# Optimization experiments

Measured on AMD Instinct MI355X. Metric: run time of the kernel, lower is better.

The kernel has to match this reference:

```python
import jax, jax.numpy as jnp
import numpy as np

B, R, D, P = 32, 512, 256, 5532  # images, rois/image, feat dim, num_pids
NEG_INF = -1e30

def setup_inputs() -> dict:
    key = jax.random.key(0)
    k1, k2, k3 = jax.random.split(key, 3)
    inputs = jax.random.normal(k1, (B * R, D), dtype=jnp.float32)
    cls_scores = jax.random.uniform(k2, (B * R, 1), dtype=jnp.float32)
    roi_label = jax.random.randint(k3, (B, R), 0, P + 1)  # 0 = background -> label -1
    return {"inputs": inputs, "cls_scores": cls_scores, "roi_label": roi_label}

def reference(inputs, cls_scores, roi_label):
    x = (inputs * cls_scores).reshape(B, R, D)          # scale features by cls score
    label = roi_label - 1                               # [B,R], -1 = background
    valid = label >= 0                                  # keep labeled ROIs only
    lbl = jnp.where(valid, label, 0)

    # per-image per-pid mean prototypes via one segmented reduction
    seg = (jnp.arange(B)[:, None] * P + lbl).reshape(-1)             # [B*R]
    w = valid.reshape(-1).astype(x.dtype)
    sums = jax.ops.segment_sum(x.reshape(-1, D) * w[:, None], seg, num_segments=B * P)
    counts = jax.ops.segment_sum(w, seg, num_segments=B * P)          # [B*P]
    proto = sums / jnp.maximum(counts, 1.0)[:, None]
    proto = proto / jnp.maximum(jnp.linalg.norm(proto, axis=-1, keepdims=True), 1e-12)
    proto = jax.lax.stop_gradient(proto).reshape(B, P, D)            # .detach() in torch
    present = (counts > 0).reshape(B, P)                              # unique labels per image

    # project each ROI feature onto its image's prototypes
    logits = jnp.einsum('brd,bpd->brp', x, proto)                     # [B,R,P]
    logits = jnp.where(present[:, None, :], logits, NEG_INF)          # softmax over unique labels only
    logp = jax.nn.log_softmax(logits, axis=-1)
    nll = -jnp.take_along_axis(logp, lbl[..., None], axis=-1)[..., 0] # [B,R]
    nll = jnp.where(valid, nll, 0.0)
    n_valid = jnp.maximum(jnp.sum(valid).astype(x.dtype), 1.0)
    return jnp.sum(nll) / n_valid
```

## Files before the change

### kernel.cpp

```cpp
#include <hip/hip_runtime.h>
#include <math.h>

#define Bn 32
#define Rn 512
#define Dn 256
#define Pn 5532
#define MAXU 512

typedef short short8 __attribute__((ext_vector_type(8)));
typedef short short4v __attribute__((ext_vector_type(4)));
typedef float floatx4 __attribute__((ext_vector_type(4)));

#define XBF_OFF    0
#define XBF_WORDS  (Bn*Rn*Dn/2)
#define PBF_OFF    (XBF_OFF + XBF_WORDS)
#define PBF_WORDS  (Bn*MAXU*Dn/2)
#define LBLC_OFF   (PBF_OFF + PBF_WORDS)
#define CCNT_OFF   (LBLC_OFF + Bn*Rn)
#define CURS_OFF   (CCNT_OFF + Bn*MAXU)
#define RLIST_OFF  (CURS_OFF + Bn*MAXU)
#define NUNIQ_OFF  (RLIST_OFF + Bn*Rn)
#define NVALID_OFF (NUNIQ_OFF + 32)
#define SEXP_OFF   (NVALID_OFF + 32)
#define NLL_OFF    (SEXP_OFF + Bn*Rn)
#define TK2_OFF    (NLL_OFF + 1)
#define TICK_OFF   (TK2_OFF + 1)
#define ZEROW      (Bn*Rn + 2 + 128)

__device__ __forceinline__ unsigned short bf16r(float f) {
    union { float f; unsigned int u; } c; c.f = f;
    return (unsigned short)((c.u + 0x7FFFu + ((c.u >> 16) & 1u)) >> 16);
}
__device__ __forceinline__ float bfu2f(unsigned int hi16) {
    union { unsigned int u; float f; } c; c.u = hi16;
    return c.f;
}

__device__ __forceinline__ void async16(void* lds, const void* g) {
    auto* l3 = reinterpret_cast<__attribute__((address_space(3))) unsigned int*>(
                   reinterpret_cast<size_t>(lds));
    auto* g1 = reinterpret_cast<const __attribute__((address_space(1))) unsigned int*>(
                   reinterpret_cast<size_t>(g));
    __builtin_amdgcn_global_load_lds(g1, l3, 16, 0, 0);
}

__global__ __launch_bounds__(1024) void k1_prep(
    const float* __restrict__ inputs, const float* __restrict__ cls,
    const int* __restrict__ roi_label,
    unsigned short* __restrict__ xbf,
    int* __restrict__ lblc_arr, int* __restrict__ ccnt, int* __restrict__ cursor,
    int* __restrict__ rlist, int* __restrict__ nuniq, int* __restrict__ nvalid_arr,
    int* __restrict__ zbase)
{
    const int flat = blockIdx.x;
    const int t = threadIdx.x;

    __shared__ int cnt_lds[Pn];
    __shared__ int cmap_lds[Pn];
    __shared__ int curs_lds[MAXU];
    __shared__ int wpres[16], wcnt[16];

    if (flat >= 32) {
        if (flat >= 33 && flat <= 49) {
            int idx = (flat - 33) * 1024 + t;
            if (idx < ZEROW) zbase[idx] = 0;
        }
        int g = (flat - 32) * 1024 + t;
        int e = g * 8;
        int row = e >> 8;
        float cw = cls[row];
        float4 v0 = *(const float4*)&inputs[e];
        float4 v1 = *(const float4*)&inputs[e + 4];
        short8 o;
        o[0] = (short)bf16r(v0.x * cw); o[1] = (short)bf16r(v0.y * cw);
        o[2] = (short)bf16r(v0.z * cw); o[3] = (short)bf16r(v0.w * cw);
        o[4] = (short)bf16r(v1.x * cw); o[5] = (short)bf16r(v1.y * cw);
        o[6] = (short)bf16r(v1.z * cw); o[7] = (short)bf16r(v1.w * cw);
        *(short8*)&xbf[e] = o;
        return;
    }

    const int b = flat;
    const int lane = t & 63, wid = t >> 6;
    for (int i = t; i < Pn; i += 1024) cnt_lds[i] = 0;
    __syncthreads();
    int mylbl = -1;
    if (t < Rn) {
        mylbl = roi_label[b * Rn + t] - 1;
        if (mylbl >= 0) atomicAdd(&cnt_lds[mylbl], 1);
    }
    __syncthreads();

    int basePres = 0, baseCnt = 0;
    for (int i0 = 0; i0 < Pn; i0 += 1024) {
        int i = i0 + t;
        int cnt = (i < Pn) ? cnt_lds[i] : 0;
        bool pres = cnt > 0;
        unsigned long long mask = __ballot(pres);
        int pfx_pres = __popcll(mask & ((1ULL << lane) - 1ULL));
        int v = cnt;
        #pragma unroll
        for (int off = 1; off < 64; off <<= 1) {
            int u = __shfl_up(v, off);
            if (lane >= off) v += u;
        }
        int pfx_cnt = v - cnt;
        if (lane == 63) { wpres[wid] = __popcll(mask); wcnt[wid] = v; }
        __syncthreads();
        int woffP = 0, totP = 0, woffC = 0, totC = 0;
        #pragma unroll
        for (int w = 0; w < 16; ++w) {
            int p = wpres[w], c = wcnt[w];
            if (w < wid) { woffP += p; woffC += c; }
            totP += p; totC += c;
        }
        if (pres) {
            int c = basePres + woffP + pfx_pres;
            cmap_lds[i] = c;
            ccnt[b * MAXU + c] = cnt;
            curs_lds[c] = baseCnt + woffC + pfx_cnt;
        }
        basePres += totP; baseCnt += totC;
        __syncthreads();
    }
    if (t < Rn) {
        int lc = (mylbl >= 0) ? cmap_lds[mylbl] : -1;
        lblc_arr[b * Rn + t] = lc;
        if (lc >= 0) {
            int pos = atomicAdd(&curs_lds[lc], 1);
            rlist[b * Rn + pos] = t;
        }
    }
    __syncthreads();
    if (t < MAXU && t < basePres)
        cursor[b * MAXU + t] = curs_lds[t];
    if (t == 0) { nuniq[b] = basePres; nvalid_arr[b] = baseCnt; }
}

__global__ __launch_bounds__(256) void k2_proto(
    const unsigned short* __restrict__ xbf,
    const int* __restrict__ nuniq, const int* __restrict__ ccnt,
    const int* __restrict__ cursor, const int* __restrict__ rlist,
    unsigned short* __restrict__ pbf)
{
    const int lane = threadIdx.x & 63, wv = threadIdx.x >> 6;
    int s = blockIdx.x * 4 + wv;
    int b = s >> 9;
    int c = s & (MAXU - 1);
    if (c >= nuniq[b]) return;
    int cnt = ccnt[s];
    int start = cursor[s] - cnt;
    float a0 = 0.f, a1 = 0.f, a2 = 0.f, a3 = 0.f;
    for (int k = 0; k < cnt; ++k) {
        int r = rlist[b * Rn + start + k];
        uint2 pk = *(const uint2*)&xbf[((size_t)(b * Rn + r)) * Dn + lane * 4];
        a0 += bfu2f(pk.x << 16); a1 += bfu2f(pk.x & 0xFFFF0000u);
        a2 += bfu2f(pk.y << 16); a3 += bfu2f(pk.y & 0xFFFF0000u);
    }
    float inv = 1.0f / (float)cnt;
    a0 *= inv; a1 *= inv; a2 *= inv; a3 *= inv;
    float ss = a0*a0 + a1*a1 + a2*a2 + a3*a3;
    #pragma unroll
    for (int off = 32; off > 0; off >>= 1) ss += __shfl_xor(ss, off);
    float scale = 1.0f / fmaxf(sqrtf(ss), 1e-12f);
    short4v o;
    o[0] = (short)bf16r(a0 * scale); o[1] = (short)bf16r(a1 * scale);
    o[2] = (short)bf16r(a2 * scale); o[3] = (short)bf16r(a3 * scale);
    *(short4v*)&pbf[(size_t)s * Dn + lane * 4] = o;
}

#define TRr 128
#define TCc 128
#define KCk 32

__global__ __launch_bounds__(256, 3) void k3_loss(
    const unsigned short* __restrict__ xbf, const unsigned short* __restrict__ pbf,
    const int* __restrict__ lblc_arr, const int* __restrict__ nuniq,
    float* __restrict__ sexp, float* __restrict__ nll,
    int* __restrict__ tick, int* __restrict__ ticket2,
    const int* __restrict__ nvalid_arr, float* __restrict__ out)
{
    __shared__ __align__(16) unsigned short xs[2][TRr * KCk];
    __shared__ __align__(16) unsigned short ps[2][TCc * KCk];
    __shared__ int lblc[TRr];
    __shared__ float msum[4];
    __shared__ int mflag;

    const int t = threadIdx.x;
    const int lane = t & 63, w = t >> 6;
    const int q = lane >> 4, r15 = lane & 15;
    const int rt = blockIdx.x;
    const int b = blockIdx.y;
    const int pc = blockIdx.z;
    const int roiBase = rt * TRr;
    const int U = nuniq[b];
    const int nch = (U == 0) ? 1 : ((U + TCc - 1) >> 7);
    if (pc >= nch) return;

    if (t < TRr) lblc[t] = lblc_arr[b * Rn + roiBase + t];

    int xrow[2], xg[2];
    #pragma unroll
    for (int cc = 0; cc < 2; ++cc) {
        int s = (w + cc * 4) * 64 + lane;
        xrow[cc] = s >> 2; xg[cc] = (s & 3) ^ ((xrow[cc] >> 1) & 3);
    }

    #define ISSUE(kc, buf)                                                         \
        do {                                                                       \
            async16(&xs[buf][w * 512],                                             \
                    xbf + (size_t)(b * Rn + roiBase + xrow[0]) * Dn                \
                        + (kc) * KCk + xg[0] * 8);                                 \
            async16(&xs[buf][(w + 4) * 512],                                       \
                    xbf + (size_t)(b * Rn + roiBase + xrow[1]) * Dn                \
                        + (kc) * KCk + xg[1] * 8);                                 \
            async16(&ps[buf][w * 512],                                             \
                    pbf + (size_t)(b * MAXU + pc * TCc + xrow[0]) * Dn             \
                        + (kc) * KCk + xg[0] * 8);                                 \
            async16(&ps[buf][(w + 4) * 512],                                       \
                    pbf + (size_t)(b * MAXU + pc * TCc + xrow[1]) * Dn             \
                        + (kc) * KCk + xg[1] * 8);                                 \
        } while (0)

    ISSUE(0, 0);

    floatx4 acc[8][2];
    #pragma unroll
    for (int mt = 0; mt < 8; ++mt)
        #pragma unroll
        for (int nt = 0; nt < 2; ++nt) acc[mt][nt] = (floatx4)0.f;

    for (int kc = 0; kc < Dn / KCk; ++kc) {
        const int cur = kc & 1;
        __syncthreads();
        if (kc < Dn / KCk - 1) ISSUE(kc + 1, cur ^ 1);

        short8 bb[2];
        #pragma unroll
        for (int nt = 0; nt < 2; ++nt) {
            int row = w * 32 + nt * 16 + r15;
            int off = row * KCk + ((q ^ ((row >> 1) & 3)) * 8);
            bb[nt] = *(const short8*)&ps[cur][off];
        }
        #pragma unroll
        for (int mt = 0; mt < 8; ++mt) {
            int row = mt * 16 + r15;
            int off = row * KCk + ((q ^ ((row >> 1) & 3)) * 8);
            short8 a = *(const short8*)&xs[cur][off];
            acc[mt][0] = __builtin_amdgcn_mfma_f32_16x16x32_bf16(a, bb[0], acc[mt][0], 0, 0, 0);
            acc[mt][1] = __builtin_amdgcn_mfma_f32_16x16x32_bf16(a, bb[1], acc[mt][1], 0, 0, 0);
        }
    }
    #undef ISSUE

    const int c0 = pc * TCc + w * 32 + r15;
    const int c1 = c0 + 16;
    const bool v0 = c0 < U, v1 = c1 < U;
    float dsum = 0.f;
    #pragma unroll
    for (int mt = 0; mt < 8; ++mt)
        #pragma unroll
        for (int reg = 0; reg < 4; ++reg) {
            int mloc = mt * 16 + q * 4 + reg;
            float d0 = acc[mt][0][reg], d1 = acc[mt][1][reg];
            int lc = lblc[mloc];
            if (v0 && c0 == lc) dsum += d0;
            if (v1 && c1 == lc) dsum += d1;
            float es = (v0 ? __expf(d0) : 0.f) + (v1 ? __expf(d1) : 0.f);
            #pragma unroll
            for (int off = 1; off < 16; off <<= 1) es += __shfl_xor(es, off);
            if (r15 == 0) atomicAdd(&sexp[b * Rn + roiBase + mloc], es);
        }
    #pragma unroll
    for (int off = 1; off < 64; off <<= 1) dsum += __shfl_xor(dsum, off);
    if (lane == 0) msum[w] = dsum;
    __syncthreads();
    if (t == 0) {
        atomicAdd(nll, -(msum[0] + msum[1] + msum[2] + msum[3]));
        __threadfence();
        int old = atomicAdd(&tick[b * 4 + rt], 1);
        mflag = (old == nch - 1);
    }
    __syncthreads();
    if (mflag) {
        float v = 0.f;
        if (t < TRr && lblc[t] >= 0)
            v = __logf(atomicAdd(&sexp[b * Rn + roiBase + t], 0.0f));
        #pragma unroll
        for (int off = 1; off < 64; off <<= 1) v += __shfl_xor(v, off);
        if (lane == 0) msum[w] = v;
        __syncthreads();
        if (t == 0) {
            atomicAdd(nll, msum[0] + msum[1] + msum[2] + msum[3]);
            __threadfence();
            int t2 = atomicAdd(ticket2, 1);
            if (t2 == 127) {
                float total = atomicAdd(nll, 0.0f);
                int nv = 0;
                for (int bb2 = 0; bb2 < Bn; ++bb2) nv += nvalid_arr[bb2];
                out[0] = total / fmaxf((float)nv, 1.0f);
            }
        }
    }
}

extern "C" void kernel_launch(void* const* d_in, const int* in_sizes, int n_in,
                              void* d_out, int out_size, void* d_ws, size_t ws_size,
                              hipStream_t stream) {
    const float* inputs = (const float*)d_in[0];
    const float* cls    = (const float*)d_in[1];
    const int*   roi    = (const int*)d_in[2];
    float* out = (float*)d_out;

    float* wsf = (float*)d_ws;
    int*   wsi = (int*)d_ws;
    unsigned short* xbf = (unsigned short*)(wsi + XBF_OFF);
    unsigned short* pbf = (unsigned short*)(wsi + PBF_OFF);
    int*   lblc   = wsi + LBLC_OFF;
    int*   ccnt   = wsi + CCNT_OFF;
    int*   cursor = wsi + CURS_OFF;
    int*   rlist  = wsi + RLIST_OFF;
    int*   nuniq  = wsi + NUNIQ_OFF;
    int*   nvalid = wsi + NVALID_OFF;
    float* sexp   = wsf + SEXP_OFF;
    float* nll    = wsf + NLL_OFF;
    int*   tk2    = wsi + TK2_OFF;
    int*   tick   = wsi + TICK_OFF;

    k1_prep<<<32 + 512, 1024, 0, stream>>>(inputs, cls, roi, xbf, lblc, ccnt,
                                           cursor, rlist, nuniq, nvalid,
                                           wsi + SEXP_OFF);
    k2_proto<<<(Bn * MAXU) / 4, 256, 0, stream>>>(xbf, nuniq, ccnt, cursor,
                                                  rlist, pbf);
    dim3 g(Rn / TRr, Bn, 4);
    k3_loss<<<g, 256, 0, stream>>>(xbf, pbf, lblc, nuniq, sexp, nll, tick, tk2,
                                   nvalid, out);
}
```

Before: 103.4 us.

## Restructure loss kernel to loop over prototype chunks with register-resident ROI tiles

The loss kernel now assigns each block 32 ROIs and loops over all prototype chunks itself, instead of splitting chunks across grid z. ROI features are loaded once into LDS and held in registers, and only prototype tiles are double-buffered. Row-wise exp sums and target logits accumulate in registers, which removes the global sexp array, its per-row atomics, the second ticket pass and most of the workspace zeroing. In exchange each block repeats the prototype loads for every 32 ROIs, and blocks for images with many unique labels run longer serial loops.

```diff
diff --git a/kernel.cpp b/kernel.cpp
--- a/kernel.cpp
+++ b/kernel.cpp
@@ -21,11 +21,9 @@
 #define RLIST_OFF  (CURS_OFF + Bn*MAXU)
 #define NUNIQ_OFF  (RLIST_OFF + Bn*Rn)
 #define NVALID_OFF (NUNIQ_OFF + 32)
-#define SEXP_OFF   (NVALID_OFF + 32)
-#define NLL_OFF    (SEXP_OFF + Bn*Rn)
-#define TK2_OFF    (NLL_OFF + 1)
-#define TICK_OFF   (TK2_OFF + 1)
-#define ZEROW      (Bn*Rn + 2 + 128)
+#define NLL_OFF    (NVALID_OFF + 32)
+#define TICK_OFF   (NLL_OFF + 1)
+#define ZEROW      2
 
 __device__ __forceinline__ unsigned short bf16r(float f) {
     union { float f; unsigned int u; } c; c.f = f;
@@ -61,10 +59,7 @@
     __shared__ int wpres[16], wcnt[16];
 
     if (flat >= 32) {
-        if (flat >= 33 && flat <= 49) {
-            int idx = (flat - 33) * 1024 + t;
-            if (idx < ZEROW) zbase[idx] = 0;
-        }
+        if (flat == 33 && t < ZEROW) zbase[t] = 0;
         int g = (flat - 32) * 1024 + t;
         int e = g * 8;
         int row = e >> 8;
@@ -169,135 +164,163 @@
     *(short4v*)&pbf[(size_t)s * Dn + lane * 4] = o;
 }
 
-#define TRr 128
+#define TRr 32
 #define TCc 128
-#define KCk 32
+#define KCs 64
+#define NSTG (Dn / KCs)
+#define NBLK ((Rn / TRr) * Bn)
 
 __global__ __launch_bounds__(256, 3) void k3_loss(
     const unsigned short* __restrict__ xbf, const unsigned short* __restrict__ pbf,
     const int* __restrict__ lblc_arr, const int* __restrict__ nuniq,
-    float* __restrict__ sexp, float* __restrict__ nll,
-    int* __restrict__ tick, int* __restrict__ ticket2,
-    const int* __restrict__ nvalid_arr, float* __restrict__ out)
+    const int* __restrict__ nvalid_arr,
+    float* __restrict__ nll, int* __restrict__ tick, float* __restrict__ out)
 {
-    __shared__ __align__(16) unsigned short xs[2][TRr * KCk];
-    __shared__ __align__(16) unsigned short ps[2][TCc * KCk];
+    __shared__ __align__(16) unsigned short xs[TRr * Dn];
+    __shared__ __align__(16) unsigned short ps[2][TCc * KCs];
     __shared__ int lblc[TRr];
-    __shared__ float msum[4];
-    __shared__ int mflag;
+    __shared__ float esum_lds[4][TRr];
+    __shared__ float dsum_lds[4][TRr];
 
     const int t = threadIdx.x;
     const int lane = t & 63, w = t >> 6;
     const int q = lane >> 4, r15 = lane & 15;
     const int rt = blockIdx.x;
-    const int b = blockIdx.y;
-    const int pc = blockIdx.z;
+    const int b  = blockIdx.y;
     const int roiBase = rt * TRr;
     const int U = nuniq[b];
-    const int nch = (U == 0) ? 1 : ((U + TCc - 1) >> 7);
-    if (pc >= nch) return;
+    const int nch = (U <= 0) ? 1 : ((U + TCc - 1) >> 7);
 
     if (t < TRr) lblc[t] = lblc_arr[b * Rn + roiBase + t];
 
-    int xrow[2], xg[2];
-    #pragma unroll
-    for (int cc = 0; cc < 2; ++cc) {
-        int s = (w + cc * 4) * 64 + lane;
-        xrow[cc] = s >> 2; xg[cc] = (s & 3) ^ ((xrow[cc] >> 1) & 3);
-    }
-
-    #define ISSUE(kc, buf)                                                         \
-        do {                                                                       \
-            async16(&xs[buf][w * 512],                                             \
-                    xbf + (size_t)(b * Rn + roiBase + xrow[0]) * Dn                \
-                        + (kc) * KCk + xg[0] * 8);                                 \
-            async16(&xs[buf][(w + 4) * 512],                                       \
-                    xbf + (size_t)(b * Rn + roiBase + xrow[1]) * Dn                \
-                        + (kc) * KCk + xg[1] * 8);                                 \
-            async16(&ps[buf][w * 512],                                             \
-                    pbf + (size_t)(b * MAXU + pc * TCc + xrow[0]) * Dn             \
-                        + (kc) * KCk + xg[0] * 8);                                 \
-            async16(&ps[buf][(w + 4) * 512],                                       \
-                    pbf + (size_t)(b * MAXU + pc * TCc + xrow[1]) * Dn             \
-                        + (kc) * KCk + xg[1] * 8);                                 \
-        } while (0)
-
-    ISSUE(0, 0);
-
-    floatx4 acc[8][2];
-    #pragma unroll
-    for (int mt = 0; mt < 8; ++mt)
-        #pragma unroll
-        for (int nt = 0; nt < 2; ++nt) acc[mt][nt] = (floatx4)0.f;
-
-    for (int kc = 0; kc < Dn / KCk; ++kc) {
-        const int cur = kc & 1;
-        __syncthreads();
-        if (kc < Dn / KCk - 1) ISSUE(kc + 1, cur ^ 1);
-
-        short8 bb[2];
+    #pragma unroll
+    for (int i = 0; i < 4; ++i) {
+        int ci = i * 256 + w * 64 + lane;
+        int row = ci >> 5, gpos = ci & 31;
+        int g = gpos ^ (row & 7);
+        async16(&xs[(i * 256 + w * 64) * 8],
+                xbf + (size_t)(b * Rn + roiBase + row) * Dn + g * 8);
+    }
+
+#define ISSUE_PS(PC, ST, BUF)                                                \
+    do {                                                                     \
+        _Pragma("unroll")                                                    \
+        for (int i_ = 0; i_ < 4; ++i_) {                                     \
+            int ci_ = i_ * 256 + w * 64 + lane;                              \
+            int pr_ = ci_ >> 3, gp_ = ci_ & 7;                               \
+            int g_ = gp_ ^ (pr_ & 7);                                        \
+            async16(&ps[BUF][(i_ * 256 + w * 64) * 8],                       \
+                    pbf + (size_t)(b * MAXU + (PC) * TCc + pr_) * Dn         \
+                        + (ST) * KCs + g_ * 8);                              \
+        }                                                                    \
+    } while (0)
+
+    ISSUE_PS(0, 0, 0);
+    __syncthreads();
+
+    short8 areg[2][8];
+    #pragma unroll
+    for (int mt = 0; mt < 2; ++mt)
+        #pragma unroll
+        for (int kcs = 0; kcs < 8; ++kcs) {
+            int row = mt * 16 + r15;
+            int gpos = (kcs * 4 + q) ^ (row & 7);
+            areg[mt][kcs] = *(const short8*)&xs[row * Dn + gpos * 8];
+        }
+
+    int lcr[2][4];
+    float esum[2][4], dsum[2][4];
+    #pragma unroll
+    for (int mt = 0; mt < 2; ++mt)
+        #pragma unroll
+        for (int reg = 0; reg < 4; ++reg) {
+            lcr[mt][reg] = lblc[mt * 16 + q * 4 + reg];
+            esum[mt][reg] = 0.f; dsum[mt][reg] = 0.f;
+        }
+
+    for (int pc = 0; pc < nch; ++pc) {
+        floatx4 acc[2][2];
+        #pragma unroll
+        for (int mt = 0; mt < 2; ++mt) {
+            acc[mt][0] = (floatx4)0.f; acc[mt][1] = (floatx4)0.f;
+        }
+
+        #pragma unroll
+        for (int st = 0; st < NSTG; ++st) {
+            const int cur = st & 1;
+            __syncthreads();
+            int ns = pc * NSTG + st + 1;
+            if (ns < nch * NSTG) ISSUE_PS(ns >> 2, ns & 3, cur ^ 1);
+            #pragma unroll
+            for (int kk = 0; kk < 2; ++kk) {
+                short8 bb[2];
+                #pragma unroll
+                for (int nt = 0; nt < 2; ++nt) {
+                    int r = w * 32 + nt * 16 + r15;
+                    int gpos = (kk * 4 + q) ^ (r & 7);
+                    bb[nt] = *(const short8*)&ps[cur][r * KCs + gpos * 8];
+                }
+                #pragma unroll
+                for (int mt = 0; mt < 2; ++mt) {
+                    acc[mt][0] = __builtin_amdgcn_mfma_f32_16x16x32_bf16(
+                        areg[mt][st * 2 + kk], bb[0], acc[mt][0], 0, 0, 0);
+                    acc[mt][1] = __builtin_amdgcn_mfma_f32_16x16x32_bf16(
+                        areg[mt][st * 2 + kk], bb[1], acc[mt][1], 0, 0, 0);
+                }
+            }
+        }
+
         #pragma unroll
         for (int nt = 0; nt < 2; ++nt) {
-            int row = w * 32 + nt * 16 + r15;
-            int off = row * KCk + ((q ^ ((row >> 1) & 3)) * 8);
-            bb[nt] = *(const short8*)&ps[cur][off];
-        }
-        #pragma unroll
-        for (int mt = 0; mt < 8; ++mt) {
-            int row = mt * 16 + r15;
-            int off = row * KCk + ((q ^ ((row >> 1) & 3)) * 8);
-            short8 a = *(const short8*)&xs[cur][off];
-            acc[mt][0] = __builtin_amdgcn_mfma_f32_16x16x32_bf16(a, bb[0], acc[mt][0], 0, 0, 0);
-            acc[mt][1] = __builtin_amdgcn_mfma_f32_16x16x32_bf16(a, bb[1], acc[mt][1], 0, 0, 0);
-        }
-    }
-    #undef ISSUE
-
-    const int c0 = pc * TCc + w * 32 + r15;
-    const int c1 = c0 + 16;
-    const bool v0 = c0 < U, v1 = c1 < U;
-    float dsum = 0.f;
-    #pragma unroll
-    for (int mt = 0; mt < 8; ++mt)
+            int c = pc * TCc + w * 32 + nt * 16 + r15;
+            bool v = c < U;
+            #pragma unroll
+            for (int mt = 0; mt < 2; ++mt)
+                #pragma unroll
+                for (int reg = 0; reg < 4; ++reg) {
+                    float d = acc[mt][nt][reg];
+                    if (v) esum[mt][reg] += __expf(d);
+                    if (c == lcr[mt][reg]) dsum[mt][reg] += d;
+                }
+        }
+    }
+#undef ISSUE_PS
+
+    #pragma unroll
+    for (int mt = 0; mt < 2; ++mt)
         #pragma unroll
         for (int reg = 0; reg < 4; ++reg) {
-            int mloc = mt * 16 + q * 4 + reg;
-            float d0 = acc[mt][0][reg], d1 = acc[mt][1][reg];
-            int lc = lblc[mloc];
-            if (v0 && c0 == lc) dsum += d0;
-            if (v1 && c1 == lc) dsum += d1;
-            float es = (v0 ? __expf(d0) : 0.f) + (v1 ? __expf(d1) : 0.f);
+            float e = esum[mt][reg], d = dsum[mt][reg];
             #pragma unroll
-            for (int off = 1; off < 16; off <<= 1) es += __shfl_xor(es, off);
-            if (r15 == 0) atomicAdd(&sexp[b * Rn + roiBase + mloc], es);
-        }
-    #pragma unroll
-    for (int off = 1; off < 64; off <<= 1) dsum += __shfl_xor(dsum, off);
-    if (lane == 0) msum[w] = dsum;
-    __syncthreads();
-    if (t == 0) {
-        atomicAdd(nll, -(msum[0] + msum[1] + msum[2] + msum[3]));
-        __threadfence();
-        int old = atomicAdd(&tick[b * 4 + rt], 1);
-        mflag = (old == nch - 1);
-    }
-    __syncthreads();
-    if (mflag) {
-        float v = 0.f;
-        if (t < TRr && lblc[t] >= 0)
-            v = __logf(atomicAdd(&sexp[b * Rn + roiBase + t], 0.0f));
-        #pragma unroll
-        for (int off = 1; off < 64; off <<= 1) v += __shfl_xor(v, off);
-        if (lane == 0) msum[w] = v;
-        __syncthreads();
+            for (int off = 1; off < 16; off <<= 1) {
+                e += __shfl_xor(e, off);
+                d += __shfl_xor(d, off);
+            }
+            if (r15 == 0) {
+                int row = mt * 16 + q * 4 + reg;
+                esum_lds[w][row] = e;
+                dsum_lds[w][row] = d;
+            }
+        }
+    __syncthreads();
+    if (t < TRr) {
+        float es = esum_lds[0][t] + esum_lds[1][t] + esum_lds[2][t] + esum_lds[3][t];
+        float ds = dsum_lds[0][t] + dsum_lds[1][t] + dsum_lds[2][t] + dsum_lds[3][t];
+        float val = (lblc[t] >= 0) ? (__logf(es) - ds) : 0.f;
+        #pragma unroll
+        for (int off = 1; off < 32; off <<= 1) val += __shfl_xor(val, off);
         if (t == 0) {
-            atomicAdd(nll, msum[0] + msum[1] + msum[2] + msum[3]);
+            atomicAdd(nll, val);
             __threadfence();
-            int t2 = atomicAdd(ticket2, 1);
-            if (t2 == 127) {
+            int old = atomicAdd(tick, 1);
+            if (old == NBLK - 1) {
                 float total = atomicAdd(nll, 0.0f);
                 int nv = 0;
-                for (int bb2 = 0; bb2 < Bn; ++bb2) nv += nvalid_arr[bb2];
+                #pragma unroll
+                for (int i = 0; i < Bn / 4; ++i) {
+                    int4 vv = ((const int4*)nvalid_arr)[i];
+                    nv += vv.x + vv.y + vv.z + vv.w;
+                }
                 out[0] = total / fmaxf((float)nv, 1.0f);
             }
         }
@@ -322,17 +345,14 @@
     int*   rlist  = wsi + RLIST_OFF;
     int*   nuniq  = wsi + NUNIQ_OFF;
     int*   nvalid = wsi + NVALID_OFF;
-    float* sexp   = wsf + SEXP_OFF;
     float* nll    = wsf + NLL_OFF;
-    int*   tk2    = wsi + TK2_OFF;
     int*   tick   = wsi + TICK_OFF;
 
     k1_prep<<<32 + 512, 1024, 0, stream>>>(inputs, cls, roi, xbf, lblc, ccnt,
                                            cursor, rlist, nuniq, nvalid,
-                                           wsi + SEXP_OFF);
+                                           wsi + NLL_OFF);
     k2_proto<<<(Bn * MAXU) / 4, 256, 0, stream>>>(xbf, nuniq, ccnt, cursor,
                                                   rlist, pbf);
-    dim3 g(Rn / TRr, Bn, 4);
-    k3_loss<<<g, 256, 0, stream>>>(xbf, pbf, lblc, nuniq, sexp, nll, tick, tk2,
-                                   nvalid, out);
-}
+    dim3 g(Rn / TRr, Bn);
+    k3_loss<<<g, 256, 0, stream>>>(xbf, pbf, lblc, nuniq, nvalid, nll, tick, out);
+}
```

After: 104.9 us. Within noise of the previous version (+1.4%).
